# Performance work log

Hardware: AMD Instinct MI355X
Metric: run time of the kernel (lower is better)

The kernel has to match this reference:

```python
import jax, jax.numpy as jnp
import numpy as np
import math

B, S, HID = 2, 2048, 512
NH, NKV, HD = 8, 2, 256
ROT = 64          # partial_rotary_factor 0.25 * head_dim 256
ROPE_THETA = 10000000.0
EPS = 1e-6


def _rms_norm(x, w):
    # zero-centered RMSNorm: x / rms * (1 + w)
    rms = jnp.sqrt(jnp.mean(x * x, axis=-1, keepdims=True) + EPS)
    return x / rms * (1.0 + w)


def _partial_rope(x, cos, sin):
    # x: [B,S,H,HD]; cos/sin: [S, ROT//2]
    xr = x[..., :ROT].reshape(*x.shape[:-1], ROT // 2, 2)
    a, b = xr[..., 0], xr[..., 1]
    c = cos[None, :, None, :]
    s = sin[None, :, None, :]
    rot = jnp.stack([a * c - b * s, a * s + b * c], axis=-1).reshape(*x.shape[:-1], ROT)
    return jnp.concatenate([rot, x[..., ROT:]], axis=-1)


def setup_inputs() -> dict:
    key = jax.random.key(0)
    ks = jax.random.split(key, 6)
    x = jax.random.normal(ks[0], (B, S, HID), dtype=jnp.float32)
    # real RoPE frequencies
    inv_freq = 1.0 / (ROPE_THETA ** (np.arange(0, ROT, 2, dtype=np.float32) / ROT))
    t = np.arange(S, dtype=np.float32)
    angles = np.outer(t, inv_freq)  # [S, ROT//2]
    cos = jnp.asarray(np.cos(angles), dtype=jnp.float32)
    sin = jnp.asarray(np.sin(angles), dtype=jnp.float32)
    # additive causal mask [S,S]
    mask = jnp.where(jnp.tril(jnp.ones((S, S), dtype=bool)), 0.0, -1e9).astype(jnp.float32)
    sc = 0.02
    wq = jax.random.normal(ks[1], (HID, NH * HD), dtype=jnp.float32) * sc
    wk = jax.random.normal(ks[2], (HID, NKV * HD), dtype=jnp.float32) * sc
    wv = jax.random.normal(ks[3], (HID, NKV * HD), dtype=jnp.float32) * sc
    wo = jax.random.normal(ks[4], (NH * HD, HID), dtype=jnp.float32) * sc
    q_norm_w = jnp.zeros((HD,), dtype=jnp.float32)
    k_norm_w = jnp.zeros((HD,), dtype=jnp.float32)
    return {"x": x, "cos": cos, "sin": sin, "mask": mask,
            "wq": wq, "wk": wk, "wv": wv, "wo": wo,
            "q_norm_w": q_norm_w, "k_norm_w": k_norm_w}


def reference(x, cos, sin, mask, wq, wk, wv, wo, q_norm_w, k_norm_w):
    b, s, _ = x.shape
    groups = NH // NKV
    q = (x @ wq).reshape(b, s, NH, HD)
    k = (x @ wk).reshape(b, s, NKV, HD)
    v = (x @ wv).reshape(b, s, NKV, HD)
    q = _partial_rope(_rms_norm(q, q_norm_w), cos, sin)
    k = _partial_rope(_rms_norm(k, k_norm_w), cos, sin)
    # GQA: broadcast kv heads to NH
    k = jnp.repeat(k, groups, axis=2)  # [b,s,NH,HD]
    v = jnp.repeat(v, groups, axis=2)
    scale = math.sqrt(HD)
    scores = jnp.einsum('bqhd,bkhd->bhqk', q, k) / scale
    scores = scores + mask[None, None, :, :]
    attn = jax.nn.softmax(scores, axis=-1)
    out = jnp.einsum('bhqk,bkhd->bqhd', attn, v).reshape(b, s, NH * HD)
    return out @ wo
```

## Files before the change

### kernel.cpp

```cpp
#include <hip/hip_runtime.h>

#define S_LEN 2048
#define NHQ 8
#define NKV 2
#define HD 256
#define KVB 32

typedef __attribute__((ext_vector_type(8))) short bf16x8;
typedef __attribute__((ext_vector_type(4))) short bf16x4;
typedef __attribute__((ext_vector_type(4))) float f32x4;
typedef __attribute__((ext_vector_type(16))) float f32x16;
typedef __attribute__((ext_vector_type(4))) unsigned u32x4;

__device__ __forceinline__ short f2bf(float f) {
    unsigned u = __builtin_bit_cast(unsigned, f);
    u += 0x7FFFu + ((u >> 16) & 1u);
    return (short)(u >> 16);
}
__device__ __forceinline__ float bf2f(short s) {
    unsigned u = ((unsigned)(unsigned short)s) << 16;
    return __builtin_bit_cast(float, u);
}
__device__ __forceinline__ unsigned cvtpk(float a, float b) {
    unsigned r;
    asm("v_cvt_pk_bf16_f32 %0, %1, %2" : "=v"(r) : "v"(a), "v"(b));
    return r;
}
__device__ __forceinline__ void gload16(const short* g, short* l) {
    __builtin_amdgcn_global_load_lds((const __attribute__((address_space(1))) unsigned*)g,
                                     (__attribute__((address_space(3))) unsigned*)l, 16, 0, 0);
}
__device__ __forceinline__ float bperm(int srclane, float v) {
    return __builtin_bit_cast(float,
        __builtin_amdgcn_ds_bpermute(srclane * 4, __builtin_bit_cast(int, v)));
}

__global__ __launch_bounds__(256) void cvt_kernel(const float* __restrict__ in,
                                                  short* __restrict__ out, int n) {
    int i = (blockIdx.x * 256 + threadIdx.x) * 4;
    if (i + 3 < n) {
        float4 f = *(const float4*)(in + i);
        bf16x4 o;
        o[0] = f2bf(f.x); o[1] = f2bf(f.y); o[2] = f2bf(f.z); o[3] = f2bf(f.w);
        *(bf16x4*)(out + i) = o;
    }
}

__global__ __launch_bounds__(256) void wt_all_kernel(const float* __restrict__ wq,
                                                     const float* __restrict__ wk,
                                                     const float* __restrict__ wv,
                                                     const float* __restrict__ wo,
                                                     short* __restrict__ wfus,
                                                     short* __restrict__ wot) {
    __shared__ short tile[64][72];
    int bid = blockIdx.x;
    const float* in; short* out; int K, N, nx, base;
    if (bid < 256)      { in = wq; out = wfus;             K = 512;  N = 2048; nx = 32; base = 0;   }
    else if (bid < 320) { in = wk; out = wfus + 2048 * 512; K = 512;  N = 512;  nx = 8;  base = 256; }
    else if (bid < 384) { in = wv; out = wfus + 2560 * 512; K = 512;  N = 512;  nx = 8;  base = 320; }
    else                { in = wo; out = wot;              K = 2048; N = 512;  nx = 8;  base = 384; }
    int lb = bid - base;
    int n0 = (lb % nx) * 64, k0 = (lb / nx) * 64;
    int t = threadIdx.x;
    #pragma unroll
    for (int i = 0; i < 16; i++) {
        int flat = i * 256 + t; int r = flat >> 6, c = flat & 63;
        tile[r][c] = f2bf(in[(long)(k0 + r) * N + n0 + c]);
    }
    __syncthreads();
    #pragma unroll
    for (int i = 0; i < 16; i++) {
        int flat = i * 256 + t; int r = flat >> 6, c = flat & 63;
        out[(long)(n0 + r) * K + k0 + c] = tile[c][r];
    }
}

template<int BN, int WRITE_BF16>
__global__ __launch_bounds__(256) void gemm_bt(const short* __restrict__ A,
                                               const short* __restrict__ Bt,
                                               void* __restrict__ Cv,
                                               int M, int N, int K) {
    constexpr int NI = BN / 32;
    __shared__ short As[128 * 32];
    __shared__ short Bs[BN * 32];
    const int t = threadIdx.x;
    const int lane = t & 63, w = t >> 6;
    const int lr = lane & 15, lg = lane >> 4;
    const int m0 = blockIdx.y * 128, n0 = blockIdx.x * BN;
    const int wm = (w >> 1) * 64, wn = (w & 1) * (BN / 2);

    f32x4 acc[4][NI];
    #pragma unroll
    for (int i = 0; i < 4; i++)
        #pragma unroll
        for (int j = 0; j < NI; j++) acc[i][j] = (f32x4){0.f, 0.f, 0.f, 0.f};

    for (int k0 = 0; k0 < K; k0 += 32) {
        __syncthreads();
        #pragma unroll
        for (int r = 0; r < 2; r++) {
            int sbase = r * 2048 + w * 512;
            int srow = (sbase + lane * 8) >> 5, scol = (sbase + lane * 8) & 31;
            gload16(A + (long)(m0 + srow) * K + k0 + scol, &As[sbase]);
        }
        #pragma unroll
        for (int r = 0; r < BN / 64; r++) {
            int sbase = r * 2048 + w * 512;
            int srow = (sbase + lane * 8) >> 5, scol = (sbase + lane * 8) & 31;
            gload16(Bt + (long)(n0 + srow) * K + k0 + scol, &Bs[sbase]);
        }
        __syncthreads();
        bf16x8 af[4], bfr[NI];
        #pragma unroll
        for (int mi = 0; mi < 4; mi++)
            af[mi] = *(const bf16x8*)&As[(wm + mi * 16 + lr) * 32 + lg * 8];
        #pragma unroll
        for (int ni = 0; ni < NI; ni++)
            bfr[ni] = *(const bf16x8*)&Bs[(wn + ni * 16 + lr) * 32 + lg * 8];
        #pragma unroll
        for (int mi = 0; mi < 4; mi++)
            #pragma unroll
            for (int ni = 0; ni < NI; ni++)
                acc[mi][ni] = __builtin_amdgcn_mfma_f32_16x16x32_bf16(af[mi], bfr[ni], acc[mi][ni], 0, 0, 0);
    }
    #pragma unroll
    for (int mi = 0; mi < 4; mi++)
    #pragma unroll
    for (int ni = 0; ni < NI; ni++)
    #pragma unroll
    for (int r = 0; r < 4; r++) {
        long row = m0 + wm + mi * 16 + lg * 4 + r;
        long col = n0 + wn + ni * 16 + lr;
        float v = acc[mi][ni][r];
        if (WRITE_BF16) ((short*)Cv)[row * N + col] = f2bf(v);
        else            ((float*)Cv)[row * N + col] = v;
    }
}

__global__ __launch_bounds__(256) void norm_rope2_kernel(
    const short* __restrict__ C, short* __restrict__ qout, short* __restrict__ kout,
    const float* __restrict__ qw, const float* __restrict__ kw,
    const float* __restrict__ cosb, const float* __restrict__ sinb) {
    int bid = blockIdx.x;
    bool isQ = bid < 8192;
    int H        = isQ ? 8 : 2;
    long cofs    = isQ ? 0L : 2048L;
    const float* w = isQ ? qw : kw;
    short* out   = isQ ? qout : kout;
    long ob      = isQ ? 4194304L : 1048576L;
    long oh      = isQ ? 256L : 524288L;
    long os      = isQ ? 2048L : 256L;
    float scale  = isQ ? 0.0625f : 1.0f;
    int vec = (isQ ? bid : bid - 8192) * 4 + (threadIdx.x >> 6);
    int lane = threadIdx.x & 63;
    int token = vec / H, head = vec % H;
    int b = token / S_LEN, s = token % S_LEN;

    bf16x4 xv = *(const bf16x4*)(C + (long)token * 3072 + cofs + head * 256 + lane * 4);
    float x0 = bf2f(xv[0]), x1 = bf2f(xv[1]), x2 = bf2f(xv[2]), x3 = bf2f(xv[3]);
    float ss = x0 * x0 + x1 * x1 + x2 * x2 + x3 * x3;
    #pragma unroll
    for (int m = 1; m < 64; m <<= 1) ss += __shfl_xor(ss, m);
    float inv = rsqrtf(ss * (1.f / 256.f) + 1e-6f);

    float4 wv = *(const float4*)(w + lane * 4);
    float y0 = x0 * inv * (1.f + wv.x);
    float y1 = x1 * inv * (1.f + wv.y);
    float y2 = x2 * inv * (1.f + wv.z);
    float y3 = x3 * inv * (1.f + wv.w);

    if (lane < 16) {
        float2 c = *(const float2*)&cosb[s * 32 + lane * 2];
        float2 sn = *(const float2*)&sinb[s * 32 + lane * 2];
        float a0 = y0 * c.x - y1 * sn.x, b0 = y0 * sn.x + y1 * c.x;
        float a1 = y2 * c.y - y3 * sn.y, b1 = y2 * sn.y + y3 * c.y;
        y0 = a0; y1 = b0; y2 = a1; y3 = b1;
    }
    y0 *= scale; y1 *= scale; y2 *= scale; y3 *= scale;
    long oidx = (long)b * ob + (long)head * oh + (long)s * os + lane * 4;
    bf16x4 o; o[0] = f2bf(y0); o[1] = f2bf(y1); o[2] = f2bf(y2); o[3] = f2bf(y3);
    *(bf16x4*)(out + oidx) = o;
}

__global__ __launch_bounds__(256) void transpose_v_kernel(const short* __restrict__ C,
                                                          short* __restrict__ vr) {
    __shared__ short tile[64][65];
    int s0 = blockIdx.x * 64, d0 = blockIdx.y * 64;
    int bkv = blockIdx.z; int b = bkv >> 1, kv = bkv & 1;
    int t = threadIdx.x;
    #pragma unroll
    for (int i = 0; i < 16; i++) {
        int flat = i * 256 + t; int si = flat >> 6, di = flat & 63;
        tile[si][di] = C[(long)(b * S_LEN + s0 + si) * 3072 + 2560 + kv * 256 + d0 + di];
    }
    __syncthreads();
    #pragma unroll
    for (int i = 0; i < 16; i++) {
        int flat = i * 256 + t; int di = flat >> 6, si = flat & 63;
        vr[(long)(bkv * 256 + d0 + di) * S_LEN + s0 + si] = tile[si][di];
    }
}

__global__ __launch_bounds__(256, 2) void flash_kernel(const short* __restrict__ Q,
                                                       const short* __restrict__ Kt,
                                                       const short* __restrict__ Vt,
                                                       short* __restrict__ O) {
    __shared__ __align__(16) char smem[66048];

    int idx = blockIdx.x;
    int xcd = idx & 7, slot = idx >> 3;
    int bh = xcd * 2 + (slot & 1);
    int j  = 31 - (slot >> 1);
    int h = bh & 7, b = bh >> 3;
    int kv = h >> 2;
    int t = threadIdx.x, lane = t & 63, w = t >> 6;
    int g = w >> 1, p = w & 1;
    int ln = lane & 31, hi = lane >> 5;
    int q0 = j * 64 + g * 32;
    int qg = q0 + ln;

    const short* Kb = Kt + (long)(b * NKV + kv) * S_LEN * HD;
    const short* Vb = Vt + (long)(b * NKV + kv) * HD * S_LEN;

    bf16x8 qf[16];
    {
        const short* qrow = Q + ((long)(b * S_LEN + qg) * NHQ + h) * HD + hi * 8;
        #pragma unroll
        for (int dc = 0; dc < 16; dc++) qf[dc] = *(const bf16x8*)&qrow[dc * 16];
    }

    f32x16 acc[8];
    #pragma unroll
    for (int i = 0; i < 8; i++)
        #pragma unroll
        for (int jj = 0; jj < 16; jj++) acc[i][jj] = 0.f;
    float m = -1e30f, l = 0.f;

    auto stage = [&](int ph2) {
        #pragma unroll
        for (int pp = 0; pp < 2; pp++) {
            int k0s = (2 * ph2 + pp) * KVB;
            short* Ktile = (short*)(smem + pp * 16384);
            short* Vtile = (short*)(smem + 32768 + pp * 16384);
            #pragma unroll
            for (int c = 0; c < 4; c++) {
                int o = c * 4096 + w * 1024 + lane * 16;
                int key = o >> 9, db = o & 511;
                gload16(Kb + (long)(k0s + key) * HD + ((db ^ ((key & 7) << 4)) >> 1),
                        Ktile + (c * 4096 + w * 1024) / 2);
                int d = o >> 6, kb = o & 63;
                gload16(Vb + (long)d * S_LEN + k0s + ((kb ^ ((d & 6) << 3)) >> 1),
                        Vtile + (c * 4096 + w * 1024) / 2);
            }
        }
    };

    auto compute = [&](int k0) {
        const char* Ks = (const char*)smem + p * 16384;
        const char* Vs = (const char*)smem + 32768 + p * 16384;
        f32x16 sA, sB;
        #pragma unroll
        for (int r = 0; r < 16; r++) { sA[r] = 0.f; sB[r] = 0.f; }
        __builtin_amdgcn_s_setprio(1);
        #pragma unroll
        for (int dc = 0; dc < 16; dc += 2) {
            int kb0 = (dc * 32 + hi * 16) ^ ((ln & 7) << 4);
            int kb1 = ((dc + 1) * 32 + hi * 16) ^ ((ln & 7) << 4);
            bf16x8 kf0 = *(const bf16x8*)(Ks + ln * 512 + kb0);
            bf16x8 kf1 = *(const bf16x8*)(Ks + ln * 512 + kb1);
            sA = __builtin_amdgcn_mfma_f32_32x32x16_bf16(kf0, qf[dc],     sA, 0, 0, 0);
            sB = __builtin_amdgcn_mfma_f32_32x32x16_bf16(kf1, qf[dc + 1], sB, 0, 0, 0);
        }
        __builtin_amdgcn_s_setprio(0);
        f32x16 s;
        #pragma unroll
        for (int r = 0; r < 16; r++) s[r] = sA[r] + sB[r];

        if (k0 + KVB - 1 > q0) {
            #pragma unroll
            for (int r = 0; r < 16; r++) {
                int key_g = k0 + (r & 3) + 8 * (r >> 2) + 4 * hi;
                if (key_g > qg) s[r] = -1e30f;
            }
        }
        float mt = s[0];
        #pragma unroll
        for (int r = 1; r < 16; r++) mt = fmaxf(mt, s[r]);
        mt = fmaxf(mt, __shfl_xor(mt, 32));
        float mn = m;
        if (!__all(mt <= m + 8.f)) {
            mn = fmaxf(m, mt);
            float f = __expf(m - mn);
            m = mn;
            float fr[16];
            #pragma unroll
            for (int r = 0; r < 16; r++)
                fr[r] = bperm((r & 3) + 8 * (r >> 2) + 4 * hi, f);
            #pragma unroll
            for (int i = 0; i < 8; i++)
                #pragma unroll
                for (int r = 0; r < 16; r++) acc[i][r] *= fr[r];
            l *= f;
        }
        float pr[16], ps = 0.f;
        #pragma unroll
        for (int r = 0; r < 16; r++) { pr[r] = __expf(s[r] - mn); ps += pr[r]; }
        ps += __shfl_xor(ps, 32);
        l += ps;

        unsigned pw[8];
        #pragma unroll
        for (int kc = 0; kc < 2; kc++) {
            unsigned X = cvtpk(pr[kc * 8 + 0], pr[kc * 8 + 1]);
            unsigned Y = cvtpk(pr[kc * 8 + 4], pr[kc * 8 + 5]);
            unsigned Z = cvtpk(pr[kc * 8 + 2], pr[kc * 8 + 3]);
            unsigned W = cvtpk(pr[kc * 8 + 6], pr[kc * 8 + 7]);
            asm volatile("v_permlane32_swap_b32 %0, %1" : "+v"(X), "+v"(Y));
            asm volatile("v_permlane32_swap_b32 %0, %1" : "+v"(Z), "+v"(W));
            pw[kc * 4 + 0] = X; pw[kc * 4 + 1] = Z;
            pw[kc * 4 + 2] = Y; pw[kc * 4 + 3] = W;
        }
        u32x4 w0v = {pw[0], pw[1], pw[2], pw[3]};
        u32x4 w1v = {pw[4], pw[5], pw[6], pw[7]};
        bf16x8 pa0 = __builtin_bit_cast(bf16x8, w0v);
        bf16x8 pa1 = __builtin_bit_cast(bf16x8, w1v);

        __builtin_amdgcn_s_setprio(1);
        #pragma unroll
        for (int db = 0; db < 8; db++) {
            int drow = db * 32 + ln;
            int sw = (drow & 6) << 3;
            bf16x8 vf0 = *(const bf16x8*)(Vs + drow * 64 + ((hi * 16) ^ sw));
            bf16x8 vf1 = *(const bf16x8*)(Vs + drow * 64 + ((32 + hi * 16) ^ sw));
            acc[db] = __builtin_amdgcn_mfma_f32_32x32x16_bf16(pa0, vf0, acc[db], 0, 0, 0);
            acc[db] = __builtin_amdgcn_mfma_f32_32x32x16_bf16(pa1, vf1, acc[db], 0, 0, 0);
        }
        __builtin_amdgcn_s_setprio(0);
    };

    stage(0);
    for (int ph = 0; ph <= j; ph++) {
        asm volatile("s_waitcnt vmcnt(0)" ::: "memory");
        __builtin_amdgcn_s_barrier();
        int k0 = (2 * ph + p) * KVB;
        if (k0 <= q0 + 31) compute(k0);
        __builtin_amdgcn_s_barrier();
        if (ph < j) stage(ph + 1);
        __builtin_amdgcn_sched_barrier(0);
    }

    float* accb = (float*)smem;
    float* mlb  = (float*)(smem + 65536);
    if (p == 1) {
        #pragma unroll
        for (int db = 0; db < 8; db++)
            #pragma unroll
            for (int r = 0; r < 16; r++)
                accb[g * 8192 + (db * 16 + r) * 64 + hi * 32 + ln] = acc[db][r];
        if (hi == 0) { mlb[g * 32 + ln] = m; mlb[64 + g * 32 + ln] = l; }
    }
    __syncthreads();
    if (p == 0) {
        float m1 = mlb[g * 32 + ln], l1 = mlb[64 + g * 32 + ln];
        float M  = fmaxf(m, m1);
        float f0 = __expf(m - M), f1 = __expf(m1 - M);
        float lt = l * f0 + l1 * f1;
        float w0 = f0 / lt, w1 = f1 / lt;
        float fr0[16], fr1[16];
        #pragma unroll
        for (int r = 0; r < 16; r++) {
            int crow = (r & 3) + 8 * (r >> 2) + 4 * hi;
            fr0[r] = bperm(crow, w0);
            fr1[r] = bperm(crow, w1);
        }
        #pragma unroll
        for (int db = 0; db < 8; db++)
            #pragma unroll
            for (int r = 0; r < 16; r++) {
                float a1 = accb[g * 8192 + (db * 16 + r) * 64 + hi * 32 + ln];
                int qrow = q0 + (r & 3) + 8 * (r >> 2) + 4 * hi;
                O[(long)(b * S_LEN + qrow) * 2048 + h * HD + db * 32 + ln] =
                    f2bf(acc[db][r] * fr0[r] + a1 * fr1[r]);
            }
    }
}

extern "C" void kernel_launch(void* const* d_in, const int* in_sizes, int n_in,
                              void* d_out, int out_size, void* d_ws, size_t ws_size,
                              hipStream_t stream) {
    const float* x    = (const float*)d_in[0];
    const float* cosb = (const float*)d_in[1];
    const float* sinb = (const float*)d_in[2];
    const float* wq   = (const float*)d_in[4];
    const float* wk   = (const float*)d_in[5];
    const float* wv   = (const float*)d_in[6];
    const float* wo   = (const float*)d_in[7];
    const float* qnw  = (const float*)d_in[8];
    const float* knw  = (const float*)d_in[9];
    float* out = (float*)d_out;

    char* ws = (char*)d_ws;
    short* xb   = (short*)(ws + 0);
    short* wfus = (short*)(ws + 4194304);
    short* wot  = (short*)(ws + 7340032);
    short* C    = (short*)(ws + 9437184);
    short* ao   = (short*)(ws + 9437184);
    short* qro  = (short*)(ws + 34603008);
    short* kr   = (short*)(ws + 51380224);
    short* vr   = (short*)(ws + 55574528);

    cvt_kernel<<<2048, 256, 0, stream>>>(x, xb, 2097152);
    wt_all_kernel<<<640, 256, 0, stream>>>(wq, wk, wv, wo, wfus, wot);

    gemm_bt<128, 1><<<dim3(24, 32), 256, 0, stream>>>(xb, wfus, C, 4096, 3072, 512);

    norm_rope2_kernel<<<10240, 256, 0, stream>>>(C, qro, kr, qnw, knw, cosb, sinb);
    transpose_v_kernel<<<dim3(32, 4, 4), 256, 0, stream>>>(C, vr);

    flash_kernel<<<512, 256, 0, stream>>>(qro, kr, vr, ao);

    gemm_bt<64, 0><<<dim3(8, 32), 256, 0, stream>>>(ao, wot, out, 4096, 512, 2048);
}
```

Baseline: 190.9 us.

## Share K/V tiles across GQA heads and double-buffer the flash attention loads

Each flash block now handles all 4 query heads of one KV group for a 32-row query chunk, using 512 threads, so each K/V tile loaded into shared memory is reused by four heads instead of being reloaded per head. Staging moves to 64-key double-buffered tiles with a partial vmcnt wait, so the next tile's loads overlap compute. This drops the previous XCD-aware block ordering and the longest-first causal ordering. It also doubles LDS use to about 129KB for one block per CU, which risks lower occupancy and load imbalance across the causal chunks.

```diff
diff --git a/kernel.cpp b/kernel.cpp
--- a/kernel.cpp
+++ b/kernel.cpp
@@ -201,26 +201,45 @@
     }
 }
 
-__global__ __launch_bounds__(256, 2) void flash_kernel(const short* __restrict__ Q,
+__global__ __launch_bounds__(512, 1) void flash_kernel(const short* __restrict__ Q,
                                                        const short* __restrict__ Kt,
                                                        const short* __restrict__ Vt,
                                                        short* __restrict__ O) {
-    __shared__ __align__(16) char smem[66048];
+    __shared__ __align__(16) char smem[132096];
 
     int idx = blockIdx.x;
-    int xcd = idx & 7, slot = idx >> 3;
-    int bh = xcd * 2 + (slot & 1);
-    int j  = 31 - (slot >> 1);
-    int h = bh & 7, b = bh >> 3;
-    int kv = h >> 2;
+    int chunk = idx >> 2;
+    int bkv = idx & 3;
+    int b = bkv >> 1, kv = bkv & 1;
     int t = threadIdx.x, lane = t & 63, w = t >> 6;
-    int g = w >> 1, p = w & 1;
+    int hh = w >> 1, p = w & 1;
+    int h = kv * 4 + hh;
     int ln = lane & 31, hi = lane >> 5;
-    int q0 = j * 64 + g * 32;
+    int q0 = chunk * 32;
     int qg = q0 + ln;
 
     const short* Kb = Kt + (long)(b * NKV + kv) * S_LEN * HD;
     const short* Vb = Vt + (long)(b * NKV + kv) * HD * S_LEN;
+
+    const int nph = (chunk >> 1) + 1;
+
+    auto stage = [&](int buf, int f) {
+        int k0s = f * 64;
+        char* base = smem + buf * 65536;
+        #pragma unroll
+        for (int cc = 0; cc < 4; cc++) {
+            int o = cc * 8192 + w * 1024 + lane * 16;
+            int key = o >> 9, db = o & 511;
+            gload16(Kb + (long)(k0s + key) * HD + ((db ^ ((key & 7) << 4)) >> 1),
+                    (short*)(base + cc * 8192 + w * 1024));
+            int d = o >> 7, kb = o & 127;
+            gload16(Vb + (long)d * S_LEN + k0s + ((kb ^ ((d & 7) << 4)) >> 1),
+                    (short*)(base + 32768 + cc * 8192 + w * 1024));
+        }
+    };
+
+    stage(0, 0);
+    if (nph > 1) stage(1, 1);
 
     bf16x8 qf[16];
     {
@@ -233,31 +252,12 @@
     #pragma unroll
     for (int i = 0; i < 8; i++)
         #pragma unroll
-        for (int jj = 0; jj < 16; jj++) acc[i][jj] = 0.f;
+        for (int r = 0; r < 16; r++) acc[i][r] = 0.f;
     float m = -1e30f, l = 0.f;
 
-    auto stage = [&](int ph2) {
-        #pragma unroll
-        for (int pp = 0; pp < 2; pp++) {
-            int k0s = (2 * ph2 + pp) * KVB;
-            short* Ktile = (short*)(smem + pp * 16384);
-            short* Vtile = (short*)(smem + 32768 + pp * 16384);
-            #pragma unroll
-            for (int c = 0; c < 4; c++) {
-                int o = c * 4096 + w * 1024 + lane * 16;
-                int key = o >> 9, db = o & 511;
-                gload16(Kb + (long)(k0s + key) * HD + ((db ^ ((key & 7) << 4)) >> 1),
-                        Ktile + (c * 4096 + w * 1024) / 2);
-                int d = o >> 6, kb = o & 63;
-                gload16(Vb + (long)d * S_LEN + k0s + ((kb ^ ((d & 6) << 3)) >> 1),
-                        Vtile + (c * 4096 + w * 1024) / 2);
-            }
-        }
-    };
-
-    auto compute = [&](int k0) {
-        const char* Ks = (const char*)smem + p * 16384;
-        const char* Vs = (const char*)smem + 32768 + p * 16384;
+    auto compute = [&](int buf, int k0) {
+        const char* Ks = (const char*)smem + buf * 65536 + p * 16384;
+        const char* Vs = (const char*)smem + buf * 65536 + 32768;
         f32x16 sA, sB;
         #pragma unroll
         for (int r = 0; r < 16; r++) { sA[r] = 0.f; sB[r] = 0.f; }
@@ -329,39 +329,39 @@
         #pragma unroll
         for (int db = 0; db < 8; db++) {
             int drow = db * 32 + ln;
-            int sw = (drow & 6) << 3;
-            bf16x8 vf0 = *(const bf16x8*)(Vs + drow * 64 + ((hi * 16) ^ sw));
-            bf16x8 vf1 = *(const bf16x8*)(Vs + drow * 64 + ((32 + hi * 16) ^ sw));
+            int sw = (drow & 7) << 4;
+            bf16x8 vf0 = *(const bf16x8*)(Vs + drow * 128 + ((p * 64 + hi * 16) ^ sw));
+            bf16x8 vf1 = *(const bf16x8*)(Vs + drow * 128 + ((p * 64 + 32 + hi * 16) ^ sw));
             acc[db] = __builtin_amdgcn_mfma_f32_32x32x16_bf16(pa0, vf0, acc[db], 0, 0, 0);
             acc[db] = __builtin_amdgcn_mfma_f32_32x32x16_bf16(pa1, vf1, acc[db], 0, 0, 0);
         }
         __builtin_amdgcn_s_setprio(0);
     };
 
-    stage(0);
-    for (int ph = 0; ph <= j; ph++) {
-        asm volatile("s_waitcnt vmcnt(0)" ::: "memory");
+    for (int f = 0; f < nph; f++) {
+        if (f + 1 < nph) { asm volatile("s_waitcnt vmcnt(8)" ::: "memory"); }
+        else             { asm volatile("s_waitcnt vmcnt(0)" ::: "memory"); }
         __builtin_amdgcn_s_barrier();
-        int k0 = (2 * ph + p) * KVB;
-        if (k0 <= q0 + 31) compute(k0);
+        int k0 = f * 64 + 32 * p;
+        if (k0 <= q0 + 31) compute(f & 1, k0);
         __builtin_amdgcn_s_barrier();
-        if (ph < j) stage(ph + 1);
+        if (f + 2 < nph) stage(f & 1, f + 2);
         __builtin_amdgcn_sched_barrier(0);
     }
 
     float* accb = (float*)smem;
-    float* mlb  = (float*)(smem + 65536);
+    float* mlb  = (float*)(smem + 131072);
     if (p == 1) {
         #pragma unroll
         for (int db = 0; db < 8; db++)
             #pragma unroll
             for (int r = 0; r < 16; r++)
-                accb[g * 8192 + (db * 16 + r) * 64 + hi * 32 + ln] = acc[db][r];
-        if (hi == 0) { mlb[g * 32 + ln] = m; mlb[64 + g * 32 + ln] = l; }
+                accb[hh * 8192 + (db * 16 + r) * 64 + hi * 32 + ln] = acc[db][r];
+        if (hi == 0) { mlb[hh * 32 + ln] = m; mlb[128 + hh * 32 + ln] = l; }
     }
     __syncthreads();
     if (p == 0) {
-        float m1 = mlb[g * 32 + ln], l1 = mlb[64 + g * 32 + ln];
+        float m1 = mlb[hh * 32 + ln], l1 = mlb[128 + hh * 32 + ln];
         float M  = fmaxf(m, m1);
         float f0 = __expf(m - M), f1 = __expf(m1 - M);
         float lt = l * f0 + l1 * f1;
@@ -377,7 +377,7 @@
         for (int db = 0; db < 8; db++)
             #pragma unroll
             for (int r = 0; r < 16; r++) {
-                float a1 = accb[g * 8192 + (db * 16 + r) * 64 + hi * 32 + ln];
+                float a1 = accb[hh * 8192 + (db * 16 + r) * 64 + hi * 32 + ln];
                 int qrow = q0 + (r & 3) + 8 * (r >> 2) + 4 * hi;
                 O[(long)(b * S_LEN + qrow) * 2048 + h * HD + db * 32 + ln] =
                     f2bf(acc[db][r] * fr0[r] + a1 * fr1[r]);
@@ -417,7 +417,7 @@
     norm_rope2_kernel<<<10240, 256, 0, stream>>>(C, qro, kr, qnw, knw, cosb, sinb);
     transpose_v_kernel<<<dim3(32, 4, 4), 256, 0, stream>>>(C, vr);
 
-    flash_kernel<<<512, 256, 0, stream>>>(qro, kr, vr, ao);
+    flash_kernel<<<256, 512, 0, stream>>>(qro, kr, vr, ao);
 
     gemm_bt<64, 0><<<dim3(8, 32), 256, 0, stream>>>(ao, wot, out, 4096, 512, 2048);
 }
```

Result: slower. 208.5 us (+9.2%).
